# Kernel optimization log

Measured on AMD Instinct MI355X. Metric: run time of the kernel, lower is better.

Reference implementation:

```python
import jax, jax.numpy as jnp
import numpy as np

P = 16          # patch size
NH = 12         # num heads
DH = 64         # head dim
C = 768         # embed dim
DEPTH = 12
HID = 3072      # mlp hidden = 4*C
EPS = 1e-6


def _ln(x, g, b):
    m = x.mean(-1, keepdims=True)
    v = ((x - m) ** 2).mean(-1, keepdims=True)
    return (x - m) / jnp.sqrt(v + EPS) * g + b


def _rope_tables(seq_len, dim):
    inv_freq = 1.0 / (10000.0 ** (jnp.arange(0, dim, 2, dtype=jnp.float32) / dim))
    freqs = jnp.arange(seq_len, dtype=jnp.float32)[:, None] * inv_freq[None, :]  # [S, dim/2]
    emb = jnp.concatenate([freqs, freqs], axis=-1)  # [S, dim] (concat layout, as in source)
    return jnp.cos(emb), jnp.sin(emb)


def _apply_rope(q, k, cos, sin):
    def rot(t):  # interleaved rotate-half, exactly as torch source
        t1, t2 = t[..., ::2], t[..., 1::2]
        return jnp.stack([-t2, t1], axis=-1).reshape(t.shape)
    return q * cos + rot(q) * sin, k * cos + rot(k) * sin


def setup_inputs() -> dict:
    key = jax.random.key(0)
    ks = jax.random.split(key, 16)
    w = lambda k, shp: (jax.random.normal(k, shp, dtype=jnp.float32) * 0.02)
    inp = {
        "x": jax.random.normal(ks[0], (4, 6, 320, 320), dtype=jnp.float32),
        "conv_w": w(ks[1], (C, 3, P, P)),
        "conv_b": jnp.zeros((C,), jnp.float32),
        "ln1_g": jnp.ones((DEPTH, C), jnp.float32),
        "ln1_b": jnp.zeros((DEPTH, C), jnp.float32),
        "qkv_w": w(ks[2], (DEPTH, C, 3 * C)),
        "qkv_b": jnp.zeros((DEPTH, 3 * C), jnp.float32),
        "proj_w": w(ks[3], (DEPTH, C, C)),
        "proj_b": jnp.zeros((DEPTH, C), jnp.float32),
        "ln2_g": jnp.ones((DEPTH, C), jnp.float32),
        "ln2_b": jnp.zeros((DEPTH, C), jnp.float32),
        "fc1_w": w(ks[4], (DEPTH, C, HID)),
        "fc1_b": jnp.zeros((DEPTH, HID), jnp.float32),
        "fc2_w": w(ks[5], (DEPTH, HID, C)),
        "fc2_b": jnp.zeros((DEPTH, C), jnp.float32),
        "lnf_g": jnp.ones((C,), jnp.float32),
        "lnf_b": jnp.zeros((C,), jnp.float32),
    }
    return inp


def reference(x, conv_w, conv_b, ln1_g, ln1_b, qkv_w, qkv_b, proj_w, proj_b,
              ln2_g, ln2_b, fc1_w, fc1_b, fc2_w, fc2_b, lnf_g, lnf_b):
    B = x.shape[0]

    def embed(img):  # [B,3,H,W] -> [B, (H/P)*(W/P), C]
        y = jax.lax.conv_general_dilated(
            img, conv_w, window_strides=(P, P), padding="VALID",
            dimension_numbers=("NCHW", "OIHW", "NCHW")) + conv_b[None, :, None, None]
        b, c, hg, wg = y.shape
        return y.reshape(b, c, hg * wg).transpose(0, 2, 1)

    t = jnp.concatenate([embed(x[:, :3]), embed(x[:, 3:])], axis=1)  # [B,S,C], S=2*400=800
    S = t.shape[1]
    cos, sin = _rope_tables(S, DH)
    cos, sin = cos[None, None], sin[None, None]  # [1,1,S,DH]
    scale = DH ** -0.5

    def block(h, p):
        l1g, l1b, qw, qb, pw, pb, l2g, l2b, f1w, f1b, f2w, f2b = p
        y = _ln(h, l1g, l1b)
        qkv = (y @ qw + qb).reshape(B, S, 3, NH, DH).transpose(2, 0, 3, 1, 4)
        q, k, v = qkv[0], qkv[1], qkv[2]  # [B,NH,S,DH]
        q, k = _apply_rope(q, k, cos, sin)
        a = jax.nn.softmax(jnp.einsum("bhsd,bhtd->bhst", q, k) * scale, axis=-1)
        o = jnp.einsum("bhst,bhtd->bhsd", a, v).transpose(0, 2, 1, 3).reshape(B, S, C)
        h = h + (o @ pw + pb)
        y = _ln(h, l2g, l2b)
        h = h + (jax.nn.gelu(y @ f1w + f1b, approximate=False) @ f2w + f2b)
        return h, None

    params = (ln1_g, ln1_b, qkv_w, qkv_b, proj_w, proj_b,
              ln2_g, ln2_b, fc1_w, fc1_b, fc2_w, fc2_b)
    t, _ = jax.lax.scan(block, t, params)
    return _ln(t, lnf_g, lnf_b)
```

## Files before the change

### kernel.cpp

```cpp
#include <hip/hip_runtime.h>
#include <hip/hip_bf16.h>
#include <math.h>

#define S_LEN   800
#define SP_LEN  832
#define C_DIM   768
#define NHEAD   12
#define DHEAD   64
#define HID_DIM 3072
#define BATCH   4
#define NTOK    (BATCH * S_LEN)
#define DEPTH_N 12

using bf16x8 = __attribute__((ext_vector_type(8))) short;
using f32x4  = __attribute__((ext_vector_type(4))) float;

__device__ inline short f2bf(float x) {
    unsigned u = __builtin_bit_cast(unsigned, x);
    u += 0x7fff + ((u >> 16) & 1);
    return (short)(u >> 16);
}

typedef const __attribute__((address_space(1))) void* gas_ptr;
typedef __attribute__((address_space(3))) void* las_ptr;
__device__ inline void async_copy16(const void* g, void* l) {
    __builtin_amdgcn_global_load_lds((gas_ptr)g, (las_ptr)l, 16, 0, 0);
}

__global__ __launch_bounds__(256)
void transpose_convert_kernel(const float* __restrict__ W, short* __restrict__ Wt,
                              int K, int N) {
    __shared__ float tile[32][33];
    int k0 = blockIdx.y * 32, n0 = blockIdx.x * 32;
    int tx = threadIdx.x & 31, ty = threadIdx.x >> 5;
#pragma unroll
    for (int i = ty; i < 32; i += 8)
        tile[i][tx] = W[(size_t)(k0 + i) * N + n0 + tx];
    __syncthreads();
#pragma unroll
    for (int i = ty; i < 32; i += 8)
        Wt[(size_t)(n0 + i) * K + k0 + tx] = f2bf(tile[tx][i]);
}

__global__ void convert_bf_kernel(const float* __restrict__ a, short* __restrict__ o, int n) {
    int i = blockIdx.x * 256 + threadIdx.x;
    if (i < n) o[i] = f2bf(a[i]);
}

__global__ void im2col_kernel(const float* __restrict__ x, short* __restrict__ A) {
    int idx = blockIdx.x * 256 + threadIdx.x;
    if (idx >= NTOK * 768) return;
    int kk = idx % 768;
    int s  = (idx / 768) % S_LEN;
    int b  = idx / (768 * S_LEN);
    int c  = kk / 256;
    int i  = (kk / 16) % 16;
    int j  = kk % 16;
    int half = s / 400, ss = s % 400;
    int hg = ss / 20, wg = ss % 20;
    int ch = half * 3 + c;
    A[idx] = f2bf(x[((size_t)(b * 6 + ch) * 320 + hg * 16 + i) * 320 + wg * 16 + j]);
}

template <int BN, bool GELU, bool RES, bool OBF>
__global__ __launch_bounds__(256)
void gemm_mfma(const short* __restrict__ A, const short* __restrict__ Bt,
               const float* __restrict__ bias, const float* __restrict__ res,
               void* __restrict__ Cout, int M, int N, int K) {
    constexpr int BM = 128, BK = 32;
    constexpr int TI = (BN == 128) ? 4 : 2;
    constexpr int TJ = 4;
    constexpr int ACALLS = BM * BK / (8 * 64);
    constexpr int BCALLS = BN * BK / (8 * 64);

    __shared__ short As[BM * BK];
    __shared__ short Bs[BN * BK];

    int tid = threadIdx.x;
    int w = tid >> 6, lane = tid & 63;
    int m0 = blockIdx.y * BM, n0 = blockIdx.x * BN;

    int wr = (BN == 128) ? (w >> 1) * 64 : w * 32;
    int wc = (BN == 128) ? (w & 1) * 64 : 0;

    f32x4 acc[TI][TJ];
#pragma unroll
    for (int i = 0; i < TI; ++i)
#pragma unroll
        for (int j = 0; j < TJ; ++j)
            acc[i][j] = (f32x4){0.f, 0.f, 0.f, 0.f};

    int mrow = wr + (lane & 15);
    int ncol = wc + (lane & 15);
    int kq = (lane >> 4) * 8;

    for (int k0 = 0; k0 < K; k0 += BK) {
#pragma unroll
        for (int j = w; j < ACALLS; j += 4) {
            int c = j * 64 + lane;
            int row = c >> 2, kc = (c & 3) * 8;
            async_copy16(A + (size_t)(m0 + row) * K + k0 + kc, As + j * 512);
        }
#pragma unroll
        for (int j = w; j < BCALLS; j += 4) {
            int c = j * 64 + lane;
            int row = c >> 2, kc = (c & 3) * 8;
            async_copy16(Bt + (size_t)(n0 + row) * K + k0 + kc, Bs + j * 512);
        }
        __syncthreads();

        bf16x8 afrag[TI], bfrag[TJ];
#pragma unroll
        for (int i = 0; i < TI; ++i)
            afrag[i] = *(const bf16x8*)(As + (mrow + i * 16) * BK + kq);
#pragma unroll
        for (int j = 0; j < TJ; ++j)
            bfrag[j] = *(const bf16x8*)(Bs + (ncol + j * 16) * BK + kq);
#pragma unroll
        for (int i = 0; i < TI; ++i)
#pragma unroll
            for (int j = 0; j < TJ; ++j)
                acc[i][j] = __builtin_amdgcn_mfma_f32_16x16x32_bf16(
                    afrag[i], bfrag[j], acc[i][j], 0, 0, 0);
        __syncthreads();
    }

    int col = lane & 15;
    int rbase = (lane >> 4) * 4;
#pragma unroll
    for (int i = 0; i < TI; ++i)
#pragma unroll
        for (int j = 0; j < TJ; ++j)
#pragma unroll
            for (int r = 0; r < 4; ++r) {
                int m = m0 + wr + i * 16 + rbase + r;
                int n = n0 + wc + j * 16 + col;
                float v = acc[i][j][r] + bias[n];
                if (RES) v += res[(size_t)m * N + n];
                if (GELU) v = 0.5f * v * (1.0f + erff(v * 0.70710678118654752f));
                if (OBF) ((short*)Cout)[(size_t)m * N + n] = f2bf(v);
                else     ((float*)Cout)[(size_t)m * N + n] = v;
            }
}

template <bool OBF>
__global__ __launch_bounds__(256)
void ln_kernel(const float* __restrict__ x, const float* __restrict__ g,
               const float* __restrict__ bta, void* __restrict__ yv) {
    int row = blockIdx.x;
    const float* xr = x + (size_t)row * C_DIM;
    int tid = threadIdx.x;

    float v0 = xr[tid], v1 = xr[tid + 256], v2 = xr[tid + 512];
    float s  = v0 + v1 + v2;
    float sq = v0 * v0 + v1 * v1 + v2 * v2;
#pragma unroll
    for (int off = 32; off; off >>= 1) {
        s  += __shfl_down(s, off);
        sq += __shfl_down(sq, off);
    }
    __shared__ float red1[4], red2[4];
    __shared__ float mean_s, rstd_s;
    int wv = tid / 64, lane = tid % 64;
    if (lane == 0) { red1[wv] = s; red2[wv] = sq; }
    __syncthreads();
    if (tid == 0) {
        float S1 = red1[0] + red1[1] + red1[2] + red1[3];
        float S2 = red2[0] + red2[1] + red2[2] + red2[3];
        float m = S1 / (float)C_DIM;
        float var = S2 / (float)C_DIM - m * m;
        mean_s = m;
        rstd_s = rsqrtf(var + 1e-6f);
    }
    __syncthreads();
    float m = mean_s, r = rstd_s;
    float o0 = (v0 - m) * r * g[tid]       + bta[tid];
    float o1 = (v1 - m) * r * g[tid + 256] + bta[tid + 256];
    float o2 = (v2 - m) * r * g[tid + 512] + bta[tid + 512];
    if (OBF) {
        short* yr = (short*)yv + (size_t)row * C_DIM;
        yr[tid] = f2bf(o0); yr[tid + 256] = f2bf(o1); yr[tid + 512] = f2bf(o2);
    } else {
        float* yr = (float*)yv + (size_t)row * C_DIM;
        yr[tid] = o0; yr[tid + 256] = o1; yr[tid + 512] = o2;
    }
}

__global__ __launch_bounds__(256)
void rope_qkv_kernel(const float* __restrict__ qkv, short* __restrict__ qb,
                     short* __restrict__ kb, short* __restrict__ vtb) {
    int st = blockIdx.x;
    int bh = blockIdx.y;
    int b = bh / NHEAD, h = bh % NHEAD;
    int s0 = st * 64;

    __shared__ short vlds[64][72];

    int tid = threadIdx.x;
    int sl = tid >> 2;
    int dc = (tid & 3) * 16;
    int s = s0 + sl;

    short qo[16], ko[16];
    if (s < S_LEN) {
        const float* base = qkv + ((size_t)(b * S_LEN + s)) * (3 * C_DIM) + h * DHEAD + dc;
        float qv[16], kv[16];
#pragma unroll
        for (int i = 0; i < 16; ++i) { qv[i] = base[i]; kv[i] = base[C_DIM + i]; }
#pragma unroll
        for (int i = 0; i < 16; ++i) {
            int d = dc + i;
            float ang = (float)s * exp2f(-(float)(d & 31) * 0.41524101186092029f);
            float c = cosf(ang), sn = sinf(ang);
            float sign = (i & 1) ? 1.0f : -1.0f;
            qo[i] = f2bf((qv[i] * c + sign * qv[i ^ 1] * sn) * 0.18033688011112042f);
            ko[i] = f2bf(kv[i] * c + sign * kv[i ^ 1] * sn);
        }
#pragma unroll
        for (int i = 0; i < 16; ++i)
            vlds[sl][dc + i] = f2bf(base[2 * C_DIM + i]);
    } else {
#pragma unroll
        for (int i = 0; i < 16; ++i) { qo[i] = 0; ko[i] = 0; vlds[sl][dc + i] = 0; }
    }
    {
        short* qd = qb + ((size_t)bh * SP_LEN + s) * DHEAD + dc;
        short* kd = kb + ((size_t)bh * SP_LEN + s) * DHEAD + dc;
        *(bf16x8*)(qd)     = *(bf16x8*)(qo);
        *(bf16x8*)(qd + 8) = *(bf16x8*)(qo + 8);
        *(bf16x8*)(kd)     = *(bf16x8*)(ko);
        *(bf16x8*)(kd + 8) = *(bf16x8*)(ko + 8);
    }
    __syncthreads();
    {
        int dr = tid >> 2, sc = (tid & 3) * 16;
        short vo[16];
#pragma unroll
        for (int i = 0; i < 16; ++i) vo[i] = vlds[sc + i][dr];
        short* vd = vtb + ((size_t)bh * DHEAD + dr) * SP_LEN + s0 + sc;
        *(bf16x8*)(vd)     = *(bf16x8*)(vo);
        *(bf16x8*)(vd + 8) = *(bf16x8*)(vo + 8);
    }
}

__global__ __launch_bounds__(256)
void attn_mfma_kernel(const short* __restrict__ qb, const short* __restrict__ kb,
                      const short* __restrict__ vtb, short* __restrict__ o) {
    int qt = blockIdx.x;
    int bh = blockIdx.y;
    int b = bh / NHEAD, h = bh % NHEAD;
    int m0 = qt * 64;

    __shared__ short Qs[64 * 64];
    __shared__ short Ks[64 * 64];
    __shared__ short Vts[64 * 64];
    __shared__ short Ps[64 * 72];

    int tid = threadIdx.x;
    int w = tid >> 6, lane = tid & 63;
    int lc = lane & 15;
    int lq = lane >> 4;
    int kq = lq * 8;

    const short* qbase = qb + (size_t)bh * SP_LEN * DHEAD;
    const short* kbase = kb + (size_t)bh * SP_LEN * DHEAD;
    const short* vbase = vtb + (size_t)bh * DHEAD * SP_LEN;

    f32x4 oacc[4];
#pragma unroll
    for (int t = 0; t < 4; ++t) oacc[t] = (f32x4){0.f, 0.f, 0.f, 0.f};
    float mrow[4] = {-3.0e38f, -3.0e38f, -3.0e38f, -3.0e38f};
    float lrow[4] = {0.f, 0.f, 0.f, 0.f};

#pragma unroll
    for (int j = w; j < 8; j += 4)
        async_copy16(qbase + (size_t)m0 * DHEAD + (j * 64 + lane) * 8, Qs + j * 512);

    for (int it = 0; it < 13; ++it) {
        int kt = it * 64;
#pragma unroll
        for (int j = w; j < 8; j += 4)
            async_copy16(kbase + (size_t)kt * DHEAD + (j * 64 + lane) * 8, Ks + j * 512);
#pragma unroll
        for (int j = w; j < 8; j += 4) {
            int c = j * 64 + lane;
            int d = c >> 3, soff = (c & 7) * 8;
            async_copy16(vbase + (size_t)d * SP_LEN + kt + soff, Vts + j * 512);
        }
        __syncthreads();

        int nt = (kt + 64 <= S_LEN) ? 4 : 2;

        bf16x8 aq0 = *(const bf16x8*)(Qs + (w * 16 + lc) * 64 + kq);
        bf16x8 aq1 = *(const bf16x8*)(Qs + (w * 16 + lc) * 64 + 32 + kq);
        f32x4 sacc[4];
        for (int t = 0; t < nt; ++t) {
            bf16x8 bk0 = *(const bf16x8*)(Ks + (t * 16 + lc) * 64 + kq);
            bf16x8 bk1 = *(const bf16x8*)(Ks + (t * 16 + lc) * 64 + 32 + kq);
            f32x4 z = (f32x4){0.f, 0.f, 0.f, 0.f};
            z = __builtin_amdgcn_mfma_f32_16x16x32_bf16(aq0, bk0, z, 0, 0, 0);
            z = __builtin_amdgcn_mfma_f32_16x16x32_bf16(aq1, bk1, z, 0, 0, 0);
            sacc[t] = z;
        }

        float rmax[4];
#pragma unroll
        for (int r = 0; r < 4; ++r) {
            float m = sacc[0][r];
            for (int t = 1; t < nt; ++t) m = fmaxf(m, sacc[t][r]);
            rmax[r] = m;
        }
#pragma unroll
        for (int off = 1; off < 16; off <<= 1)
#pragma unroll
            for (int r = 0; r < 4; ++r)
                rmax[r] = fmaxf(rmax[r], __shfl_xor(rmax[r], off));

        float alpha[4], rsum[4] = {0.f, 0.f, 0.f, 0.f};
#pragma unroll
        for (int r = 0; r < 4; ++r) {
            float mnew = fmaxf(mrow[r], rmax[r]);
            alpha[r] = exp2f(mrow[r] - mnew);
            mrow[r] = mnew;
        }
        for (int t = 0; t < nt; ++t) {
#pragma unroll
            for (int r = 0; r < 4; ++r) {
                float p = exp2f(sacc[t][r] - mrow[r]);
                rsum[r] += p;
                Ps[(w * 16 + lq * 4 + r) * 72 + t * 16 + lc] = f2bf(p);
            }
        }
#pragma unroll
        for (int off = 1; off < 16; off <<= 1)
#pragma unroll
            for (int r = 0; r < 4; ++r)
                rsum[r] += __shfl_xor(rsum[r], off);
#pragma unroll
        for (int r = 0; r < 4; ++r) lrow[r] = lrow[r] * alpha[r] + rsum[r];

#pragma unroll
        for (int t = 0; t < 4; ++t)
#pragma unroll
            for (int r = 0; r < 4; ++r) oacc[t][r] *= alpha[r];

        int nk = nt >> 1;
        for (int kstep = 0; kstep < nk; ++kstep) {
            bf16x8 ap = *(const bf16x8*)(Ps + (w * 16 + lc) * 72 + kstep * 32 + kq);
#pragma unroll
            for (int t = 0; t < 4; ++t) {
                bf16x8 bv = *(const bf16x8*)(Vts + (t * 16 + lc) * 64 + kstep * 32 + kq);
                oacc[t] = __builtin_amdgcn_mfma_f32_16x16x32_bf16(ap, bv, oacc[t], 0, 0, 0);
            }
        }
        __syncthreads();
    }

    float inv_l[4];
#pragma unroll
    for (int r = 0; r < 4; ++r) inv_l[r] = 1.0f / lrow[r];
#pragma unroll
    for (int t = 0; t < 4; ++t)
#pragma unroll
        for (int r = 0; r < 4; ++r) {
            int row = w * 16 + lq * 4 + r;
            int s = m0 + row;
            if (s < S_LEN) {
                int n = t * 16 + lc;
                o[((size_t)(b * S_LEN + s)) * C_DIM + h * DHEAD + n] = f2bf(oacc[t][r] * inv_l[r]);
            }
        }
}

extern "C" void kernel_launch(void* const* d_in, const int* in_sizes, int n_in,
                              void* d_out, int out_size, void* d_ws, size_t ws_size,
                              hipStream_t stream) {
    const float* x      = (const float*)d_in[0];
    const float* conv_w = (const float*)d_in[1];
    const float* conv_b = (const float*)d_in[2];
    const float* ln1_g  = (const float*)d_in[3];
    const float* ln1_b  = (const float*)d_in[4];
    const float* qkv_w  = (const float*)d_in[5];
    const float* qkv_b  = (const float*)d_in[6];
    const float* proj_w = (const float*)d_in[7];
    const float* proj_b = (const float*)d_in[8];
    const float* ln2_g  = (const float*)d_in[9];
    const float* ln2_b  = (const float*)d_in[10];
    const float* fc1_w  = (const float*)d_in[11];
    const float* fc1_b  = (const float*)d_in[12];
    const float* fc2_w  = (const float*)d_in[13];
    const float* fc2_b  = (const float*)d_in[14];
    const float* lnf_g  = (const float*)d_in[15];
    const float* lnf_b  = (const float*)d_in[16];

    const size_t NTC = (size_t)NTOK * C_DIM;
    const size_t HSD = (size_t)BATCH * NHEAD * SP_LEN * DHEAD;
    float* ws = (float*)d_ws;
    float* h       = ws;
    float* qkv_out = h + NTC;
    short* qb      = (short*)(qkv_out + (size_t)NTOK * 3 * C_DIM);
    short* kb      = qb + HSD;
    short* vtb     = kb + HSD;
    short* y_bf    = vtb + HSD;
    short* big_bf  = y_bf + NTC;
    short* wbuf    = big_bf + (size_t)NTOK * HID_DIM;
    short* embed_wt = wbuf + (size_t)HID_DIM * C_DIM;

    convert_bf_kernel<<<(768 * 768 + 255) / 256, 256, 0, stream>>>(conv_w, embed_wt, 768 * 768);
    im2col_kernel<<<(NTOK * 768 + 255) / 256, 256, 0, stream>>>(x, big_bf);
    gemm_mfma<64, false, false, false><<<dim3(C_DIM / 64, NTOK / 128), 256, 0, stream>>>(
        big_bf, embed_wt, conv_b, nullptr, h, NTOK, C_DIM, C_DIM);

    for (int l = 0; l < DEPTH_N; ++l) {
        const float* l1g = ln1_g + (size_t)l * C_DIM;
        const float* l1b = ln1_b + (size_t)l * C_DIM;
        const float* qw  = qkv_w + (size_t)l * C_DIM * 3 * C_DIM;
        const float* qbs = qkv_b + (size_t)l * 3 * C_DIM;
        const float* pw  = proj_w + (size_t)l * C_DIM * C_DIM;
        const float* pb  = proj_b + (size_t)l * C_DIM;
        const float* l2g = ln2_g + (size_t)l * C_DIM;
        const float* l2b = ln2_b + (size_t)l * C_DIM;
        const float* f1w = fc1_w + (size_t)l * C_DIM * HID_DIM;
        const float* f1b = fc1_b + (size_t)l * HID_DIM;
        const float* f2w = fc2_w + (size_t)l * HID_DIM * C_DIM;
        const float* f2b = fc2_b + (size_t)l * C_DIM;

        ln_kernel<true><<<NTOK, 256, 0, stream>>>(h, l1g, l1b, y_bf);
        transpose_convert_kernel<<<dim3(3 * C_DIM / 32, C_DIM / 32), 256, 0, stream>>>(
            qw, wbuf, C_DIM, 3 * C_DIM);
        gemm_mfma<128, false, false, false><<<dim3(3 * C_DIM / 128, NTOK / 128), 256, 0, stream>>>(
            y_bf, wbuf, qbs, nullptr, qkv_out, NTOK, 3 * C_DIM, C_DIM);

        rope_qkv_kernel<<<dim3(13, BATCH * NHEAD), 256, 0, stream>>>(qkv_out, qb, kb, vtb);
        attn_mfma_kernel<<<dim3(13, BATCH * NHEAD), 256, 0, stream>>>(qb, kb, vtb, y_bf);

        transpose_convert_kernel<<<dim3(C_DIM / 32, C_DIM / 32), 256, 0, stream>>>(
            pw, wbuf, C_DIM, C_DIM);
        gemm_mfma<64, false, true, false><<<dim3(C_DIM / 64, NTOK / 128), 256, 0, stream>>>(
            y_bf, wbuf, pb, h, h, NTOK, C_DIM, C_DIM);

        ln_kernel<true><<<NTOK, 256, 0, stream>>>(h, l2g, l2b, y_bf);
        transpose_convert_kernel<<<dim3(HID_DIM / 32, C_DIM / 32), 256, 0, stream>>>(
            f1w, wbuf, C_DIM, HID_DIM);
        gemm_mfma<128, true, false, true><<<dim3(HID_DIM / 128, NTOK / 128), 256, 0, stream>>>(
            y_bf, wbuf, f1b, nullptr, big_bf, NTOK, HID_DIM, C_DIM);
        transpose_convert_kernel<<<dim3(C_DIM / 32, HID_DIM / 32), 256, 0, stream>>>(
            f2w, wbuf, HID_DIM, C_DIM);
        gemm_mfma<64, false, true, false><<<dim3(C_DIM / 64, NTOK / 128), 256, 0, stream>>>(
            big_bf, wbuf, f2b, h, h, NTOK, C_DIM, HID_DIM);
    }

    ln_kernel<false><<<NTOK, 256, 0, stream>>>(h, lnf_g, lnf_b, d_out);
}
```

Measured before the change: 2.990 ms.

## Widen GEMM K-tile with XOR-swizzled LDS, bf16 QKV, larger attention key tiles

The GEMM K tile grows from 32 to 64, and the LDS layout uses an XOR swizzle on 16-byte chunks to avoid bank conflicts on fragment reads. The QKV GEMM now writes bf16 instead of fp32, which halves its store traffic and lets the rope kernel use vector loads. The attention kernel handles 128 keys per iteration with swizzled K and V^T tiles, and the sequence padding grows to 896 to fit. This cuts loop and barrier overhead and memory traffic, at the cost of more LDS per block and rounding QKV to bf16 before rope.

```diff
diff --git a/kernel.cpp b/kernel.cpp
--- a/kernel.cpp
+++ b/kernel.cpp
@@ -3,7 +3,7 @@
 #include <math.h>
 
 #define S_LEN   800
-#define SP_LEN  832
+#define SP_LEN  896
 #define C_DIM   768
 #define NHEAD   12
 #define DHEAD   64
@@ -19,6 +19,10 @@
     unsigned u = __builtin_bit_cast(unsigned, x);
     u += 0x7fff + ((u >> 16) & 1);
     return (short)(u >> 16);
+}
+__device__ inline float bf2f(short x) {
+    unsigned u = ((unsigned)(unsigned short)x) << 16;
+    return __builtin_bit_cast(float, u);
 }
 
 typedef const __attribute__((address_space(1))) void* gas_ptr;
@@ -67,14 +71,14 @@
 void gemm_mfma(const short* __restrict__ A, const short* __restrict__ Bt,
                const float* __restrict__ bias, const float* __restrict__ res,
                void* __restrict__ Cout, int M, int N, int K) {
-    constexpr int BM = 128, BK = 32;
+    constexpr int BM = 128, BK = 64;
     constexpr int TI = (BN == 128) ? 4 : 2;
     constexpr int TJ = 4;
     constexpr int ACALLS = BM * BK / (8 * 64);
     constexpr int BCALLS = BN * BK / (8 * 64);
 
-    __shared__ short As[BM * BK];
-    __shared__ short Bs[BN * BK];
+    __shared__ __align__(16) short As[BM * BK];
+    __shared__ __align__(16) short Bs[BN * BK];
 
     int tid = threadIdx.x;
     int w = tid >> 6, lane = tid & 63;
@@ -90,43 +94,47 @@
         for (int j = 0; j < TJ; ++j)
             acc[i][j] = (f32x4){0.f, 0.f, 0.f, 0.f};
 
-    int mrow = wr + (lane & 15);
-    int ncol = wc + (lane & 15);
-    int kq = (lane >> 4) * 8;
+    int lc = lane & 15, lq = lane >> 4;
 
     for (int k0 = 0; k0 < K; k0 += BK) {
 #pragma unroll
         for (int j = w; j < ACALLS; j += 4) {
             int c = j * 64 + lane;
-            int row = c >> 2, kc = (c & 3) * 8;
-            async_copy16(A + (size_t)(m0 + row) * K + k0 + kc, As + j * 512);
+            int row = c >> 3, p = c & 7, q = p ^ (row & 7);
+            async_copy16(A + (size_t)(m0 + row) * K + k0 + q * 8, As + j * 512);
         }
 #pragma unroll
         for (int j = w; j < BCALLS; j += 4) {
             int c = j * 64 + lane;
-            int row = c >> 2, kc = (c & 3) * 8;
-            async_copy16(Bt + (size_t)(n0 + row) * K + k0 + kc, Bs + j * 512);
+            int row = c >> 3, p = c & 7, q = p ^ (row & 7);
+            async_copy16(Bt + (size_t)(n0 + row) * K + k0 + q * 8, Bs + j * 512);
         }
         __syncthreads();
 
-        bf16x8 afrag[TI], bfrag[TJ];
-#pragma unroll
-        for (int i = 0; i < TI; ++i)
-            afrag[i] = *(const bf16x8*)(As + (mrow + i * 16) * BK + kq);
-#pragma unroll
-        for (int j = 0; j < TJ; ++j)
-            bfrag[j] = *(const bf16x8*)(Bs + (ncol + j * 16) * BK + kq);
-#pragma unroll
-        for (int i = 0; i < TI; ++i)
-#pragma unroll
-            for (int j = 0; j < TJ; ++j)
-                acc[i][j] = __builtin_amdgcn_mfma_f32_16x16x32_bf16(
-                    afrag[i], bfrag[j], acc[i][j], 0, 0, 0);
+#pragma unroll
+        for (int h = 0; h < 2; ++h) {
+            bf16x8 afrag[TI], bfrag[TJ];
+#pragma unroll
+            for (int i = 0; i < TI; ++i) {
+                int row = wr + i * 16 + lc;
+                afrag[i] = *(const bf16x8*)(As + row * 64 + ((((h << 2) | lq)) ^ (row & 7)) * 8);
+            }
+#pragma unroll
+            for (int j = 0; j < TJ; ++j) {
+                int col = wc + j * 16 + lc;
+                bfrag[j] = *(const bf16x8*)(Bs + col * 64 + ((((h << 2) | lq)) ^ (col & 7)) * 8);
+            }
+#pragma unroll
+            for (int i = 0; i < TI; ++i)
+#pragma unroll
+                for (int j = 0; j < TJ; ++j)
+                    acc[i][j] = __builtin_amdgcn_mfma_f32_16x16x32_bf16(
+                        afrag[i], bfrag[j], acc[i][j], 0, 0, 0);
+        }
         __syncthreads();
     }
 
-    int col = lane & 15;
-    int rbase = (lane >> 4) * 4;
+    int rbase = lq * 4;
 #pragma unroll
     for (int i = 0; i < TI; ++i)
 #pragma unroll
@@ -134,7 +142,7 @@
 #pragma unroll
             for (int r = 0; r < 4; ++r) {
                 int m = m0 + wr + i * 16 + rbase + r;
-                int n = n0 + wc + j * 16 + col;
+                int n = n0 + wc + j * 16 + lc;
                 float v = acc[i][j][r] + bias[n];
                 if (RES) v += res[(size_t)m * N + n];
                 if (GELU) v = 0.5f * v * (1.0f + erff(v * 0.70710678118654752f));
@@ -187,14 +195,14 @@
 }
 
 __global__ __launch_bounds__(256)
-void rope_qkv_kernel(const float* __restrict__ qkv, short* __restrict__ qb,
+void rope_qkv_kernel(const short* __restrict__ qkv, short* __restrict__ qb,
                      short* __restrict__ kb, short* __restrict__ vtb) {
     int st = blockIdx.x;
     int bh = blockIdx.y;
     int b = bh / NHEAD, h = bh % NHEAD;
     int s0 = st * 64;
 
-    __shared__ short vlds[64][72];
+    __shared__ __align__(16) short vlds[64][72];
 
     int tid = threadIdx.x;
     int sl = tid >> 2;
@@ -203,10 +211,17 @@
 
     short qo[16], ko[16];
     if (s < S_LEN) {
-        const float* base = qkv + ((size_t)(b * S_LEN + s)) * (3 * C_DIM) + h * DHEAD + dc;
+        const short* base = qkv + ((size_t)(b * S_LEN + s)) * (3 * C_DIM) + h * DHEAD + dc;
+        short qsh[16], ksh[16], vsh[16];
+        *(bf16x8*)(qsh)     = *(const bf16x8*)(base);
+        *(bf16x8*)(qsh + 8) = *(const bf16x8*)(base + 8);
+        *(bf16x8*)(ksh)     = *(const bf16x8*)(base + C_DIM);
+        *(bf16x8*)(ksh + 8) = *(const bf16x8*)(base + C_DIM + 8);
+        *(bf16x8*)(vsh)     = *(const bf16x8*)(base + 2 * C_DIM);
+        *(bf16x8*)(vsh + 8) = *(const bf16x8*)(base + 2 * C_DIM + 8);
         float qv[16], kv[16];
 #pragma unroll
-        for (int i = 0; i < 16; ++i) { qv[i] = base[i]; kv[i] = base[C_DIM + i]; }
+        for (int i = 0; i < 16; ++i) { qv[i] = bf2f(qsh[i]); kv[i] = bf2f(ksh[i]); }
 #pragma unroll
         for (int i = 0; i < 16; ++i) {
             int d = dc + i;
@@ -216,9 +231,8 @@
             qo[i] = f2bf((qv[i] * c + sign * qv[i ^ 1] * sn) * 0.18033688011112042f);
             ko[i] = f2bf(kv[i] * c + sign * kv[i ^ 1] * sn);
         }
-#pragma unroll
-        for (int i = 0; i < 16; ++i)
-            vlds[sl][dc + i] = f2bf(base[2 * C_DIM + i]);
+        *(bf16x8*)&vlds[sl][dc]     = *(bf16x8*)(vsh);
+        *(bf16x8*)&vlds[sl][dc + 8] = *(bf16x8*)(vsh + 8);
     } else {
 #pragma unroll
         for (int i = 0; i < 16; ++i) { qo[i] = 0; ko[i] = 0; vlds[sl][dc + i] = 0; }
@@ -251,15 +265,14 @@
     int b = bh / NHEAD, h = bh % NHEAD;
     int m0 = qt * 64;
 
-    __shared__ short Qs[64 * 64];
-    __shared__ short Ks[64 * 64];
-    __shared__ short Vts[64 * 64];
-    __shared__ short Ps[64 * 72];
+    __shared__ __align__(16) short Qs[64 * 64];
+    __shared__ __align__(16) short Ks[128 * 64];
+    __shared__ __align__(16) short Vts[64 * 128];
+    __shared__ __align__(16) short Ps[64 * 136];
 
     int tid = threadIdx.x;
     int w = tid >> 6, lane = tid & 63;
-    int lc = lane & 15;
-    int lq = lane >> 4;
+    int lc = lane & 15, lq = lane >> 4;
     int kq = lq * 8;
 
     const short* qbase = qb + (size_t)bh * SP_LEN * DHEAD;
@@ -273,30 +286,39 @@
     float lrow[4] = {0.f, 0.f, 0.f, 0.f};
 
 #pragma unroll
-    for (int j = w; j < 8; j += 4)
-        async_copy16(qbase + (size_t)m0 * DHEAD + (j * 64 + lane) * 8, Qs + j * 512);
-
-    for (int it = 0; it < 13; ++it) {
-        int kt = it * 64;
-#pragma unroll
-        for (int j = w; j < 8; j += 4)
-            async_copy16(kbase + (size_t)kt * DHEAD + (j * 64 + lane) * 8, Ks + j * 512);
-#pragma unroll
-        for (int j = w; j < 8; j += 4) {
+    for (int j = w; j < 8; j += 4) {
+        int c = j * 64 + lane;
+        int row = c >> 3, p = c & 7, q = p ^ (row & 7);
+        async_copy16(qbase + (size_t)(m0 + row) * DHEAD + q * 8, Qs + j * 512);
+    }
+
+    for (int it = 0; it < 7; ++it) {
+        int kt = it * 128;
+#pragma unroll
+        for (int j = w; j < 16; j += 4) {
             int c = j * 64 + lane;
-            int d = c >> 3, soff = (c & 7) * 8;
-            async_copy16(vbase + (size_t)d * SP_LEN + kt + soff, Vts + j * 512);
+            int row = c >> 3, p = c & 7, q = p ^ (row & 7);
+            async_copy16(kbase + (size_t)(kt + row) * DHEAD + q * 8, Ks + j * 512);
+        }
+#pragma unroll
+        for (int j = w; j < 16; j += 4) {
+            int c = j * 64 + lane;
+            int d = c >> 4, p = c & 15, sq = p ^ (d & 15);
+            async_copy16(vbase + (size_t)d * SP_LEN + kt + sq * 8, Vts + j * 512);
         }
         __syncthreads();
 
-        int nt = (kt + 64 <= S_LEN) ? 4 : 2;
-
-        bf16x8 aq0 = *(const bf16x8*)(Qs + (w * 16 + lc) * 64 + kq);
-        bf16x8 aq1 = *(const bf16x8*)(Qs + (w * 16 + lc) * 64 + 32 + kq);
-        f32x4 sacc[4];
+        int nt = (it < 6) ? 8 : 2;
+
+        int qrow = w * 16 + lc;
+        bf16x8 aq0 = *(const bf16x8*)(Qs + qrow * 64 + ((lq) ^ (qrow & 7)) * 8);
+        bf16x8 aq1 = *(const bf16x8*)(Qs + qrow * 64 + ((4 | lq) ^ (qrow & 7)) * 8);
+
+        f32x4 sacc[8];
         for (int t = 0; t < nt; ++t) {
-            bf16x8 bk0 = *(const bf16x8*)(Ks + (t * 16 + lc) * 64 + kq);
-            bf16x8 bk1 = *(const bf16x8*)(Ks + (t * 16 + lc) * 64 + 32 + kq);
+            int kr = t * 16 + lc;
+            bf16x8 bk0 = *(const bf16x8*)(Ks + kr * 64 + ((lq) ^ (kr & 7)) * 8);
+            bf16x8 bk1 = *(const bf16x8*)(Ks + kr * 64 + ((4 | lq) ^ (kr & 7)) * 8);
             f32x4 z = (f32x4){0.f, 0.f, 0.f, 0.f};
             z = __builtin_amdgcn_mfma_f32_16x16x32_bf16(aq0, bk0, z, 0, 0, 0);
             z = __builtin_amdgcn_mfma_f32_16x16x32_bf16(aq1, bk1, z, 0, 0, 0);
@@ -328,7 +350,7 @@
             for (int r = 0; r < 4; ++r) {
                 float p = exp2f(sacc[t][r] - mrow[r]);
                 rsum[r] += p;
-                Ps[(w * 16 + lq * 4 + r) * 72 + t * 16 + lc] = f2bf(p);
+                Ps[(w * 16 + lq * 4 + r) * 136 + t * 16 + lc] = f2bf(p);
             }
         }
 #pragma unroll
@@ -338,18 +360,18 @@
                 rsum[r] += __shfl_xor(rsum[r], off);
 #pragma unroll
         for (int r = 0; r < 4; ++r) lrow[r] = lrow[r] * alpha[r] + rsum[r];
-
 #pragma unroll
         for (int t = 0; t < 4; ++t)
 #pragma unroll
             for (int r = 0; r < 4; ++r) oacc[t][r] *= alpha[r];
 
-        int nk = nt >> 1;
+        int nk = (nt == 8) ? 4 : 1;
         for (int kstep = 0; kstep < nk; ++kstep) {
-            bf16x8 ap = *(const bf16x8*)(Ps + (w * 16 + lc) * 72 + kstep * 32 + kq);
+            bf16x8 ap = *(const bf16x8*)(Ps + (w * 16 + lc) * 136 + kstep * 32 + kq);
 #pragma unroll
             for (int t = 0; t < 4; ++t) {
-                bf16x8 bv = *(const bf16x8*)(Vts + (t * 16 + lc) * 64 + kstep * 32 + kq);
+                int dr = t * 16 + lc;
+                bf16x8 bv = *(const bf16x8*)(Vts + dr * 128 + ((((kstep << 2) | lq)) ^ (dr & 15)) * 8);
                 oacc[t] = __builtin_amdgcn_mfma_f32_16x16x32_bf16(ap, bv, oacc[t], 0, 0, 0);
             }
         }
@@ -397,8 +419,8 @@
     const size_t HSD = (size_t)BATCH * NHEAD * SP_LEN * DHEAD;
     float* ws = (float*)d_ws;
     float* h       = ws;
-    float* qkv_out = h + NTC;
-    short* qb      = (short*)(qkv_out + (size_t)NTOK * 3 * C_DIM);
+    short* qkv_bf  = (short*)(h + NTC);
+    short* qb      = qkv_bf + (size_t)NTOK * 3 * C_DIM;
     short* kb      = qb + HSD;
     short* vtb     = kb + HSD;
     short* y_bf    = vtb + HSD;
@@ -428,10 +450,10 @@
         ln_kernel<true><<<NTOK, 256, 0, stream>>>(h, l1g, l1b, y_bf);
         transpose_convert_kernel<<<dim3(3 * C_DIM / 32, C_DIM / 32), 256, 0, stream>>>(
             qw, wbuf, C_DIM, 3 * C_DIM);
-        gemm_mfma<128, false, false, false><<<dim3(3 * C_DIM / 128, NTOK / 128), 256, 0, stream>>>(
-            y_bf, wbuf, qbs, nullptr, qkv_out, NTOK, 3 * C_DIM, C_DIM);
-
-        rope_qkv_kernel<<<dim3(13, BATCH * NHEAD), 256, 0, stream>>>(qkv_out, qb, kb, vtb);
+        gemm_mfma<128, false, false, true><<<dim3(3 * C_DIM / 128, NTOK / 128), 256, 0, stream>>>(
+            y_bf, wbuf, qbs, nullptr, qkv_bf, NTOK, 3 * C_DIM, C_DIM);
+
+        rope_qkv_kernel<<<dim3(14, BATCH * NHEAD), 256, 0, stream>>>(qkv_bf, qb, kb, vtb);
         attn_mfma_kernel<<<dim3(13, BATCH * NHEAD), 256, 0, stream>>>(qb, kb, vtb, y_bf);
 
         transpose_convert_kernel<<<dim3(C_DIM / 32, C_DIM / 32), 256, 0, stream>>>(
```

After: 2.799 ms. -6.4%, faster.
